# Performance work log

Measured on AMD Instinct MI355X. Metric: run time of the kernel, lower is better.

The kernel has to match this reference:

```python
import jax, jax.numpy as jnp
import numpy as np

N = 50000      # nodes
E = 800000     # edges
FEAT = 128     # input feature dim
EMB = 256      # embed_dim = heads * hid
H = 4          # attention heads
C = 64         # hid_dim per head
PED = 32       # positional encoding dim
NEG_SLOPE = 0.2


def setup_inputs() -> dict:
    key = jax.random.key(0)
    ks = jax.random.split(key, 20)
    s = lambda i, shape, sc=0.1: jax.random.normal(ks[i], shape, jnp.float32) * sc
    return {
        "x": s(0, (N, FEAT), 1.0),
        "x_masked": s(1, (N, FEAT), 1.0),
        "PE": s(2, (N, PED), 1.0),
        "PE_noise": s(3, (N, PED), 1.0),
        "edge_index": jax.random.randint(ks[4], (2, E), 0, N),
        # PEG positional encoder (linear + relu)
        "W_peg": s(5, (PED, PED)), "b_peg": jnp.zeros((PED,), jnp.float32),
        # GAT layer 0
        "W0": s(6, (FEAT, H * C)), "a_s0": s(7, (H, C)), "a_d0": s(8, (H, C)),
        "w_pe0": s(9, (H,)), "W_u0": s(10, (PED, PED)),
        # GAT layer 1
        "W1": s(11, (EMB, H * C)), "a_s1": s(12, (H, C)), "a_d1": s(13, (H, C)),
        "w_pe1": s(14, (H,)), "W_u1": s(15, (PED, PED)),
    }


def _gat(x, pe, src, dst, W, a_s, a_d, w_pe, W_u):
    # PE-aware GATConv: standard GAT attention + PE-distance bias per head.
    xp = (x @ W).reshape(-1, H, C)                       # [N,H,C]
    al_s = (xp * a_s).sum(-1)                            # [N,H]
    al_d = (xp * a_d).sum(-1)                            # [N,H]
    dist = jnp.sqrt(((pe[src] - pe[dst]) ** 2).sum(-1) + 1e-8)   # [E]
    logits = jax.nn.leaky_relu(al_s[src] + al_d[dst], NEG_SLOPE) \
             + dist[:, None] * w_pe                      # [E,H]
    # segment softmax over incoming edges of each dst node
    m = jax.ops.segment_max(logits, dst, num_segments=N)
    e = jnp.exp(logits - m[dst])
    den = jax.ops.segment_sum(e, dst, num_segments=N)
    alpha = e / (den[dst] + 1e-16)                       # [E,H]
    out = jax.ops.segment_sum(alpha[:, :, None] * xp[src], dst,
                              num_segments=N).reshape(-1, H * C)  # [N,H*C]
    pe_out = jax.nn.relu(pe @ W_u)                       # per-layer PE update
    return out, pe_out


def reference(x, x_masked, PE, PE_noise, W_peg, b_peg,
              W0, a_s0, a_d0, w_pe0, W_u0,
              W1, a_s1, a_d1, w_pe1, W_u1, edge_index):
    src, dst = edge_index[0], edge_index[1]
    # PEG encoder on both PE branches
    pe = jax.nn.relu(PE @ W_peg + b_peg)
    pe_n = jax.nn.relu(PE_noise @ W_peg + b_peg)
    # layer 0 (dual branches; eval mode -> dropout is identity)
    h, pe_n = _gat(x, pe_n, src, dst, W0, a_s0, a_d0, w_pe0, W_u0)
    hm, pe = _gat(x_masked, pe, src, dst, W0, a_s0, a_d0, w_pe0, W_u0)
    h = jax.nn.relu(h)
    hm = jax.nn.relu(hm)
    # layer 1 (last layer: no activation)
    h, pe_n = _gat(h, pe_n, src, dst, W1, a_s1, a_d1, w_pe1, W_u1)
    hm, pe = _gat(hm, pe, src, dst, W1, a_s1, a_d1, w_pe1, W_u1)
    return (hm, pe_n)
```

## Files before the change

### kernel.cpp

```cpp
#include <hip/hip_runtime.h>
#include <hip/hip_bf16.h>

#define N_NODES 50000
#define N_EDGES 800000
#define NEG_SLOPE 0.2f

typedef __hip_bfloat16 bf16;
typedef __attribute__((ext_vector_type(8))) short short8;
typedef __attribute__((ext_vector_type(4))) float f32x4;

__device__ __forceinline__ float b2f(bf16 x) { return __bfloat162float(x); }

__device__ __forceinline__ float ldsel(const void* p, size_t i, int isbf) {
  return isbf ? __bfloat162float(((const bf16*)p)[i]) : ((const float*)p)[i];
}
__device__ __forceinline__ void stsel(void* p, size_t i, int isbf, float v) {
  if (isbf) ((bf16*)p)[i] = __float2bfloat16(v);
  else ((float*)p)[i] = v;
}

__global__ void detect_kernel(const unsigned short* __restrict__ probe,
                              int* __restrict__ flag) {
  if (threadIdx.x == 0 && blockIdx.x == 0) {
    int weird = 0;
    for (int i = 0; i < 512; i += 2) {
      int ex = (probe[i] >> 7) & 0xFF;
      if (ex >= 0x85) weird++;
    }
    *flag = (weird < 8) ? 1 : 0;
  }
}

struct CvtJobs {
  const void* src[10];
  float* dst[10];
  int n[10];
};
__global__ __launch_bounds__(256) void cvt_kernel(CvtJobs jobs, const int* __restrict__ flag) {
  int isbf = *flag;
  for (int j = 0; j < 10; j++) {
    int n = jobs.n[j];
    const void* s = jobs.src[j];
    float* d = jobs.dst[j];
    for (int i = blockIdx.x * 256 + threadIdx.x; i < n; i += gridDim.x * 256)
      d[i] = ldsel(s, i, isbf);
  }
}

template <int K>
__global__ __launch_bounds__(256) void transpose_cvt_kernel(const void* __restrict__ in,
                                                            bf16* __restrict__ out,
                                                            const int* __restrict__ flag) {
  int isbf = *flag;
  int i = blockIdx.x * 256 + threadIdx.x;
  if (i >= 256 * K) return;
  int n = i / K, k = i - n * K;
  out[i] = __float2bfloat16(ldsel(in, (size_t)k * 256 + n, isbf));
}

__global__ __launch_bounds__(256) void peg_chain3(const void* __restrict__ in,
                                                  const float* __restrict__ Wpeg,
                                                  const float* __restrict__ bpeg,
                                                  const float* __restrict__ Wu0,
                                                  const float* __restrict__ Wu1,
                                                  void* out, size_t out_off,
                                                  const int* __restrict__ flag) {
  __shared__ float w1[1024], w2[1024], w3[1024];
  __shared__ float rowA[256], rowB[256];
  int isbf = *flag;
  int tid = threadIdx.x;
  int n0 = blockIdx.x * 8;
  for (int i = tid; i < 1024; i += 256) {
    w1[i] = Wpeg[i];
    w2[i] = Wu0[i];
    w3[i] = Wu1[i];
  }
  rowA[tid] = ldsel(in, (size_t)n0 * 32 + tid, isbf);
  __syncthreads();
  int col = tid & 31, ln = tid >> 5;
  float acc = bpeg[col];
#pragma unroll
  for (int j = 0; j < 32; j++) acc += rowA[ln * 32 + j] * w1[j * 32 + col];
  rowB[tid] = fmaxf(acc, 0.f);
  __syncthreads();
  acc = 0.f;
#pragma unroll
  for (int j = 0; j < 32; j++) acc += rowB[ln * 32 + j] * w2[j * 32 + col];
  rowA[tid] = fmaxf(acc, 0.f);
  __syncthreads();
  acc = 0.f;
#pragma unroll
  for (int j = 0; j < 32; j++) acc += rowA[ln * 32 + j] * w3[j * 32 + col];
  stsel(out, out_off + (size_t)n0 * 32 + tid, isbf, fmaxf(acc, 0.f));
}

__global__ __launch_bounds__(256) void peg_chain2(const void* __restrict__ in,
                                                  const float* __restrict__ Wpeg,
                                                  const float* __restrict__ bpeg,
                                                  const float* __restrict__ Wu0,
                                                  bf16* __restrict__ pe0,
                                                  bf16* __restrict__ pe1,
                                                  const int* __restrict__ flag) {
  __shared__ float w1[1024], w2[1024];
  __shared__ float rowA[256], rowB[256];
  int isbf = *flag;
  int tid = threadIdx.x;
  int n0 = blockIdx.x * 8;
  for (int i = tid; i < 1024; i += 256) {
    w1[i] = Wpeg[i];
    w2[i] = Wu0[i];
  }
  rowA[tid] = ldsel(in, (size_t)n0 * 32 + tid, isbf);
  __syncthreads();
  int col = tid & 31, ln = tid >> 5;
  float acc = bpeg[col];
#pragma unroll
  for (int j = 0; j < 32; j++) acc += rowA[ln * 32 + j] * w1[j * 32 + col];
  acc = fmaxf(acc, 0.f);
  pe0[(size_t)n0 * 32 + tid] = __float2bfloat16(acc);
  rowB[tid] = acc;
  __syncthreads();
  acc = 0.f;
#pragma unroll
  for (int j = 0; j < 32; j++) acc += rowB[ln * 32 + j] * w2[j * 32 + col];
  pe1[(size_t)n0 * 32 + tid] = __float2bfloat16(fmaxf(acc, 0.f));
}

template <int K, bool A_DUAL>
__global__ __launch_bounds__(256) void mfma_gemm(const void* __restrict__ Ap,
                                                 const bf16* __restrict__ Bt,
                                                 bf16* __restrict__ C, int M,
                                                 const float* __restrict__ a_sf,
                                                 const float* __restrict__ a_df,
                                                 float* __restrict__ al_s,
                                                 float* __restrict__ al_d,
                                                 const int* __restrict__ flag) {
  constexpr int LDK = 136;
  __shared__ short a_lds[64 * LDK];
  __shared__ short b_lds[64 * LDK];
  __shared__ float lds_al[128];
  int nrt = (M + 63) / 64;
  int bid = blockIdx.x;
  int xcd = bid & 7;
  int jj = bid >> 3;
  int col_t = jj & 3;
  int row_t = (jj >> 2) * 8 + xcd;
  if (row_t >= nrt) return;
  int isbf = A_DUAL ? *flag : 1;
  int tid = threadIdx.x;
  int row0 = row_t * 64;
  int col0 = col_t * 64;
  int lane = tid & 63;
  int wv = tid >> 6;
  int wm = (wv & 1) * 32, wn = (wv >> 1) * 32;
  int l15 = lane & 15, quad = lane >> 4;
  if (tid < 128) lds_al[tid] = 0.f;
  f32x4 acc00 = {0.f, 0.f, 0.f, 0.f}, acc01 = acc00, acc10 = acc00, acc11 = acc00;

  for (int kb = 0; kb < K; kb += 128) {
    if (kb) __syncthreads();
    for (int idx = tid; idx < 64 * 16; idx += 256) {
      int r = idx >> 4, sidx = idx & 15;
      int gr = row0 + r;
      size_t gi = (size_t)gr * K + kb + sidx * 8;
      uint4 av = make_uint4(0u, 0u, 0u, 0u);
      if (A_DUAL && !isbf) {
        if (gr < M) {
          float4 f0 = ((const float4*)Ap)[gi / 4];
          float4 f1 = ((const float4*)Ap)[gi / 4 + 1];
          union { uint4 v; bf16 h[8]; } o;
          o.h[0] = __float2bfloat16(f0.x);
          o.h[1] = __float2bfloat16(f0.y);
          o.h[2] = __float2bfloat16(f0.z);
          o.h[3] = __float2bfloat16(f0.w);
          o.h[4] = __float2bfloat16(f1.x);
          o.h[5] = __float2bfloat16(f1.y);
          o.h[6] = __float2bfloat16(f1.z);
          o.h[7] = __float2bfloat16(f1.w);
          av = o.v;
        }
      } else {
        if (gr < M) av = *(const uint4*)&((const bf16*)Ap)[gi];
      }
      *(uint4*)&a_lds[r * LDK + sidx * 8] = av;
      *(uint4*)&b_lds[r * LDK + sidx * 8] =
          *(const uint4*)&Bt[(size_t)(col0 + r) * K + kb + sidx * 8];
    }
    __syncthreads();
#pragma unroll
    for (int k0 = 0; k0 < 128; k0 += 32) {
      int ko = k0 + quad * 8;
      short8 a0 = *(const short8*)&a_lds[(wm + l15) * LDK + ko];
      short8 a1 = *(const short8*)&a_lds[(wm + 16 + l15) * LDK + ko];
      short8 b0 = *(const short8*)&b_lds[(wn + l15) * LDK + ko];
      short8 b1 = *(const short8*)&b_lds[(wn + 16 + l15) * LDK + ko];
      acc00 = __builtin_amdgcn_mfma_f32_16x16x32_bf16(a0, b0, acc00, 0, 0, 0);
      acc01 = __builtin_amdgcn_mfma_f32_16x16x32_bf16(a0, b1, acc01, 0, 0, 0);
      acc10 = __builtin_amdgcn_mfma_f32_16x16x32_bf16(a1, b0, acc10, 0, 0, 0);
      acc11 = __builtin_amdgcn_mfma_f32_16x16x32_bf16(a1, b1, acc11, 0, 0, 0);
    }
  }
  const f32x4* accs[2][2] = {{&acc00, &acc01}, {&acc10, &acc11}};
  float as0 = a_sf[col0 + wn + l15], as1 = a_sf[col0 + wn + 16 + l15];
  float ad0 = a_df[col0 + wn + l15], ad1 = a_df[col0 + wn + 16 + l15];
#pragma unroll
  for (int i = 0; i < 2; i++) {
    float sp[4], dp[4];
#pragma unroll
    for (int r = 0; r < 4; r++) {
      float v0 = (*accs[i][0])[r], v1 = (*accs[i][1])[r];
      sp[r] = v0 * as0 + v1 * as1;
      dp[r] = v0 * ad0 + v1 * ad1;
      int grow = row0 + wm + i * 16 + quad * 4 + r;
      if (grow < M) {
        C[(size_t)grow * 256 + col0 + wn + l15] = __float2bfloat16(v0);
        C[(size_t)grow * 256 + col0 + wn + 16 + l15] = __float2bfloat16(v1);
      }
    }
#pragma unroll
    for (int off = 1; off < 16; off <<= 1) {
#pragma unroll
      for (int r = 0; r < 4; r++) {
        sp[r] += __shfl_xor(sp[r], off);
        dp[r] += __shfl_xor(dp[r], off);
      }
    }
    if (l15 == 0) {
#pragma unroll
      for (int r = 0; r < 4; r++) {
        int lrow = wm + i * 16 + quad * 4 + r;
        atomicAdd(&lds_al[lrow], sp[r]);
        atomicAdd(&lds_al[64 + lrow], dp[r]);
      }
    }
  }
  __syncthreads();
  if (tid < 64 && row0 + tid < M) {
    al_s[(size_t)(row0 + tid) * 4 + col_t] = lds_al[tid];
    al_d[(size_t)(row0 + tid) * 4 + col_t] = lds_al[64 + tid];
  }
}

__global__ __launch_bounds__(256) void hist_kernel(const int* __restrict__ dst,
                                                   int* __restrict__ deg) {
  int e = blockIdx.x * 256 + threadIdx.x;
  atomicAdd(&deg[dst[e]], 1);
}

__global__ __launch_bounds__(1024) void scan1_kernel(const int* __restrict__ deg,
                                                     int* __restrict__ tmp,
                                                     int* __restrict__ bsum, int n) {
  __shared__ int wsum[16];
  int tid = threadIdx.x;
  int idx = blockIdx.x * 1024 + tid;
  int v = (idx < n) ? deg[idx] : 0;
  int incl = v;
#pragma unroll
  for (int off = 1; off < 64; off <<= 1) {
    int t = __shfl_up(incl, off);
    if ((tid & 63) >= off) incl += t;
  }
  int wid = tid >> 6;
  if ((tid & 63) == 63) wsum[wid] = incl;
  __syncthreads();
  if (tid == 0) {
    int acc = 0;
#pragma unroll
    for (int w = 0; w < 16; w++) {
      int t = wsum[w];
      wsum[w] = acc;
      acc += t;
    }
    bsum[blockIdx.x] = acc;
  }
  __syncthreads();
  if (idx < n) tmp[idx] = wsum[wid] + incl;
}

__global__ void scan2_kernel(int* __restrict__ bsum, int nb) {
  int tid = threadIdx.x;
  int v = (tid < nb) ? bsum[tid] : 0;
  int incl = v;
#pragma unroll
  for (int off = 1; off < 64; off <<= 1) {
    int t = __shfl_up(incl, off);
    if (tid >= off) incl += t;
  }
  if (tid < nb) bsum[tid] = incl - v;
}

__global__ __launch_bounds__(1024) void scan3_kernel(const int* __restrict__ tmp,
                                                     const int* __restrict__ bsum,
                                                     int* __restrict__ rowptr, int n) {
  int idx = blockIdx.x * 1024 + threadIdx.x;
  if (idx < n) rowptr[idx + 1] = tmp[idx] + bsum[blockIdx.x];
  if (idx == 0) rowptr[0] = 0;
}

__global__ __launch_bounds__(256) void fill_kernel(const int* __restrict__ src,
                                                   const int* __restrict__ dst,
                                                   const int* __restrict__ rowptr,
                                                   int* __restrict__ fill,
                                                   int* __restrict__ csr_src) {
  int e = blockIdx.x * 256 + threadIdx.x;
  int d = dst[e];
  int pos = atomicAdd(&fill[d], 1);
  csr_src[rowptr[d] + pos] = src[e];
}

template <bool RELU, bool OUT_DUAL>
__global__ __launch_bounds__(256) void agg_kernel(const bf16* __restrict__ xp,
                                                  const bf16* __restrict__ pe,
                                                  const float* __restrict__ al_s,
                                                  const float* __restrict__ al_d,
                                                  const float* __restrict__ w_pe,
                                                  const int* __restrict__ csr_src,
                                                  const int* __restrict__ rowptr,
                                                  void* out, const int* __restrict__ flag) {
  int isbf = OUT_DUAL ? *flag : 1;
  int lane = threadIdx.x & 63;
  int n = blockIdx.x * 4 + (threadIdx.x >> 6);
  int q = lane >> 4, li = lane & 15, h = li >> 2;
  unsigned int ud = *(const unsigned int*)&pe[(size_t)n * 32 + li * 2];
  float pdlo = __uint_as_float(ud << 16);
  float pdhi = __uint_as_float(ud & 0xffff0000u);
  float ald = al_d[(size_t)n * 4 + h];
  float wph = w_pe[h];
  int s1 = rowptr[n + 1];
  int s = rowptr[n] + q;
  float acc[16];
#pragma unroll
  for (int j = 0; j < 16; j++) acc[j] = 0.f;
  float asum = 0.f;

  int sn_c = -1, sn_n = -1;
  unsigned int pes_c = 0, pes_n = 0;
  float als_c = 0.f, als_n = 0.f;
  uint4 xc0 = make_uint4(0u, 0u, 0u, 0u), xc1 = xc0;
  uint4 xn0 = xc0, xn1 = xc0;
  if (s < s1) {
    sn_c = csr_src[s];
    pes_c = *(const unsigned int*)&pe[(size_t)sn_c * 32 + li * 2];
    als_c = al_s[(size_t)sn_c * 4 + h];
    const uint4* b = (const uint4*)&xp[(size_t)sn_c * 256 + li * 16];
    xc0 = b[0];
    xc1 = b[1];
    if (s + 4 < s1) sn_n = csr_src[s + 4];
  }
  int sf = s + 8;
  while (sn_c >= 0) {
    if (sn_n >= 0) {
      pes_n = *(const unsigned int*)&pe[(size_t)sn_n * 32 + li * 2];
      als_n = al_s[(size_t)sn_n * 4 + h];
      const uint4* b = (const uint4*)&xp[(size_t)sn_n * 256 + li * 16];
      xn0 = b[0];
      xn1 = b[1];
    }
    int sn_f = (sf < s1) ? csr_src[sf] : -1;
    sf += 4;
    float dx = __uint_as_float(pes_c << 16) - pdlo;
    float dy = __uint_as_float(pes_c & 0xffff0000u) - pdhi;
    float d2 = dx * dx + dy * dy;
#pragma unroll
    for (int off = 1; off < 16; off <<= 1) d2 += __shfl_xor(d2, off);
    float lg = als_c + ald;
    lg = (lg >= 0.f) ? lg : NEG_SLOPE * lg;
    lg += sqrtf(d2 + 1e-8f) * wph;
    float a = __expf(lg);
    unsigned int u[8] = {xc0.x, xc0.y, xc0.z, xc0.w, xc1.x, xc1.y, xc1.z, xc1.w};
#pragma unroll
    for (int p = 0; p < 8; p++) {
      acc[2 * p] += a * __uint_as_float(u[p] << 16);
      acc[2 * p + 1] += a * __uint_as_float(u[p] & 0xffff0000u);
    }
    asum += a;
    sn_c = sn_n;
    pes_c = pes_n;
    als_c = als_n;
    xc0 = xn0;
    xc1 = xn1;
    sn_n = sn_f;
  }
#pragma unroll
  for (int j = 0; j < 16; j++) {
    acc[j] += __shfl_xor(acc[j], 16);
    acc[j] += __shfl_xor(acc[j], 32);
  }
  asum += __shfl_xor(asum, 16);
  asum += __shfl_xor(asum, 32);
  if (q == 0) {
    float inv = 1.f / (asum + 1e-16f);
    size_t oi = (size_t)n * 256 + li * 16;
    if (OUT_DUAL && !isbf) {
      float* of = (float*)out;
#pragma unroll
      for (int p = 0; p < 4; p++) {
        float4 f;
        f.x = acc[4 * p] * inv;
        f.y = acc[4 * p + 1] * inv;
        f.z = acc[4 * p + 2] * inv;
        f.w = acc[4 * p + 3] * inv;
        if (RELU) {
          f.x = fmaxf(f.x, 0.f);
          f.y = fmaxf(f.y, 0.f);
          f.z = fmaxf(f.z, 0.f);
          f.w = fmaxf(f.w, 0.f);
        }
        *(float4*)&of[oi + 4 * p] = f;
      }
    } else {
      union { uint4 v[2]; bf16 hh[16]; } o;
#pragma unroll
      for (int j = 0; j < 16; j++) {
        float r = acc[j] * inv;
        if (RELU) r = fmaxf(r, 0.f);
        o.hh[j] = __float2bfloat16(r);
      }
      uint4* ob = (uint4*)&((bf16*)out)[oi];
      ob[0] = o.v[0];
      ob[1] = o.v[1];
    }
  }
}

extern "C" void kernel_launch(void* const* d_in, const int* in_sizes, int n_in,
                              void* d_out, int out_size, void* d_ws, size_t ws_size,
                              hipStream_t stream) {
  const void* x_masked = d_in[1];
  const void* PE = d_in[2];
  const void* PE_noise = d_in[3];
  const int* ei = (const int*)d_in[4];
  const int* src = ei;
  const int* dst = ei + N_EDGES;

  char* w = (char*)d_ws;
  auto alloc = [&](size_t bytes) -> char* {
    char* p = w;
    w += (bytes + 255) / 256 * 256;
    return p;
  };
  int* flag = (int*)alloc(4);
  float* W_peg_f = (float*)alloc(1024 * 4);
  float* b_peg_f = (float*)alloc(32 * 4);
  float* a_s0_f = (float*)alloc(256 * 4);
  float* a_d0_f = (float*)alloc(256 * 4);
  float* w_pe0_f = (float*)alloc(4 * 4);
  float* W_u0_f = (float*)alloc(1024 * 4);
  float* a_s1_f = (float*)alloc(256 * 4);
  float* a_d1_f = (float*)alloc(256 * 4);
  float* w_pe1_f = (float*)alloc(4 * 4);
  float* W_u1_f = (float*)alloc(1024 * 4);
  bf16* Wt0 = (bf16*)alloc(32768 * 2);
  bf16* Wt1 = (bf16*)alloc(65536 * 2);
  bf16* pe0_bf = (bf16*)alloc((size_t)N_NODES * 32 * 2);
  bf16* pe1_bf = (bf16*)alloc((size_t)N_NODES * 32 * 2);
  float* al_s = (float*)alloc((size_t)N_NODES * 4 * 4);
  float* al_d = (float*)alloc((size_t)N_NODES * 4 * 4);
  int* degfill = (int*)alloc((size_t)N_NODES * 2 * 4);
  int* deg = degfill;
  int* fill = degfill + N_NODES;
  int* rowptr = (int*)alloc((size_t)(N_NODES + 1) * 4);
  int* stmp = (int*)alloc((size_t)N_NODES * 4);
  int* bsum = (int*)alloc(64 * 4);
  int* csr_src = (int*)alloc((size_t)N_EDGES * 4);
  bf16* xp = (bf16*)alloc((size_t)N_NODES * 256 * 2);
  bf16* hm0 = (bf16*)alloc((size_t)N_NODES * 256 * 2);

  detect_kernel<<<1, 64, 0, stream>>>((const unsigned short*)d_in[5], flag);
  CvtJobs jobs;
  int ji = 0;
  auto addjob = [&](const void* s, float* d, int n) {
    jobs.src[ji] = s; jobs.dst[ji] = d; jobs.n[ji] = n; ji++;
  };
  addjob(d_in[5], W_peg_f, 1024);
  addjob(d_in[6], b_peg_f, 32);
  addjob(d_in[8], a_s0_f, 256);
  addjob(d_in[9], a_d0_f, 256);
  addjob(d_in[10], w_pe0_f, 4);
  addjob(d_in[11], W_u0_f, 1024);
  addjob(d_in[13], a_s1_f, 256);
  addjob(d_in[14], a_d1_f, 256);
  addjob(d_in[15], w_pe1_f, 4);
  addjob(d_in[16], W_u1_f, 1024);
  cvt_kernel<<<16, 256, 0, stream>>>(jobs, flag);
  transpose_cvt_kernel<128><<<128, 256, 0, stream>>>(d_in[7], Wt0, flag);
  transpose_cvt_kernel<256><<<256, 256, 0, stream>>>(d_in[12], Wt1, flag);

  hipMemsetAsync(degfill, 0, (size_t)N_NODES * 2 * 4, stream);

  hist_kernel<<<N_EDGES / 256, 256, 0, stream>>>(dst, deg);
  scan1_kernel<<<49, 1024, 0, stream>>>(deg, stmp, bsum, N_NODES);
  scan2_kernel<<<1, 64, 0, stream>>>(bsum, 49);
  scan3_kernel<<<49, 1024, 0, stream>>>(stmp, bsum, rowptr, N_NODES);
  fill_kernel<<<N_EDGES / 256, 256, 0, stream>>>(src, dst, rowptr, fill, csr_src);

  peg_chain3<<<N_NODES / 8, 256, 0, stream>>>(PE_noise, W_peg_f, b_peg_f, W_u0_f, W_u1_f,
                                              d_out, (size_t)N_NODES * 256, flag);
  peg_chain2<<<N_NODES / 8, 256, 0, stream>>>(PE, W_peg_f, b_peg_f, W_u0_f, pe0_bf, pe1_bf, flag);

  int nrt = (N_NODES + 63) / 64;
  int gblk = ((nrt + 7) / 8) * 8 * 4;

  mfma_gemm<128, true><<<gblk, 256, 0, stream>>>(x_masked, Wt0, xp, N_NODES,
                                                 a_s0_f, a_d0_f, al_s, al_d, flag);
  agg_kernel<true, false><<<N_NODES / 4, 256, 0, stream>>>(
      xp, pe0_bf, al_s, al_d, w_pe0_f, csr_src, rowptr, hm0, flag);

  mfma_gemm<256, false><<<gblk, 256, 0, stream>>>(hm0, Wt1, xp, N_NODES,
                                                  a_s1_f, a_d1_f, al_s, al_d, flag);
  agg_kernel<false, true><<<N_NODES / 4, 256, 0, stream>>>(
      xp, pe1_bf, al_s, al_d, w_pe1_f, csr_src, rowptr, d_out, flag);
}
```

Measured before the change: 470.3 us.

## Merge setup and PEG kernels, unroll aggregation loop two edges per step

Folds the dtype-detection, weight conversion and two transpose kernels into a single prep kernel, with each block running its own detection. The two PEG chain kernels become one launch that branches on block index. The aggregation loop now processes two edges per iteration with a double-buffered prefetch, using a -1e30 logit so out-of-range slots contribute zero weight. The goal is fewer kernel launches and more memory-level parallelism in the gather, at the cost of more registers and redundant detection work in every prep block.

```diff
diff --git a/kernel.cpp b/kernel.cpp
--- a/kernel.cpp
+++ b/kernel.cpp
@@ -19,16 +19,16 @@
   else ((float*)p)[i] = v;
 }
 
-__global__ void detect_kernel(const unsigned short* __restrict__ probe,
-                              int* __restrict__ flag) {
-  if (threadIdx.x == 0 && blockIdx.x == 0) {
-    int weird = 0;
-    for (int i = 0; i < 512; i += 2) {
-      int ex = (probe[i] >> 7) & 0xFF;
-      if (ex >= 0x85) weird++;
-    }
-    *flag = (weird < 8) ? 1 : 0;
-  }
+__device__ __forceinline__ int block_detect(const unsigned short* __restrict__ probe) {
+  __shared__ int wcount;
+  int tid = threadIdx.x;
+  if (tid == 0) wcount = 0;
+  __syncthreads();
+  int ex = (probe[2 * tid] >> 7) & 0xFF;
+  unsigned long long m = __ballot(ex >= 0x85);
+  if ((tid & 63) == 0) atomicAdd(&wcount, __popcll(m));
+  __syncthreads();
+  return wcount < 8;
 }
 
 struct CvtJobs {
@@ -36,44 +36,57 @@
   float* dst[10];
   int n[10];
 };
-__global__ __launch_bounds__(256) void cvt_kernel(CvtJobs jobs, const int* __restrict__ flag) {
-  int isbf = *flag;
-  for (int j = 0; j < 10; j++) {
-    int n = jobs.n[j];
-    const void* s = jobs.src[j];
-    float* d = jobs.dst[j];
-    for (int i = blockIdx.x * 256 + threadIdx.x; i < n; i += gridDim.x * 256)
-      d[i] = ldsel(s, i, isbf);
-  }
-}
-
-template <int K>
-__global__ __launch_bounds__(256) void transpose_cvt_kernel(const void* __restrict__ in,
-                                                            bf16* __restrict__ out,
-                                                            const int* __restrict__ flag) {
-  int isbf = *flag;
-  int i = blockIdx.x * 256 + threadIdx.x;
-  if (i >= 256 * K) return;
-  int n = i / K, k = i - n * K;
-  out[i] = __float2bfloat16(ldsel(in, (size_t)k * 256 + n, isbf));
-}
-
-__global__ __launch_bounds__(256) void peg_chain3(const void* __restrict__ in,
-                                                  const float* __restrict__ Wpeg,
-                                                  const float* __restrict__ bpeg,
-                                                  const float* __restrict__ Wu0,
-                                                  const float* __restrict__ Wu1,
-                                                  void* out, size_t out_off,
-                                                  const int* __restrict__ flag) {
+__global__ __launch_bounds__(256) void prep_kernel(CvtJobs jobs,
+                                                   const unsigned short* __restrict__ probe,
+                                                   const void* __restrict__ W0in,
+                                                   bf16* __restrict__ Wt0,
+                                                   const void* __restrict__ W1in,
+                                                   bf16* __restrict__ Wt1,
+                                                   int* __restrict__ flag) {
+  int tid = threadIdx.x;
+  int isbf = block_detect(probe);
+  int b = blockIdx.x;
+  if (b == 0 && tid == 0) *flag = isbf;
+  if (b < 16) {
+    for (int j = 0; j < 10; j++) {
+      int n = jobs.n[j];
+      const void* s = jobs.src[j];
+      float* d = jobs.dst[j];
+      for (int i = b * 256 + tid; i < n; i += 16 * 256) d[i] = ldsel(s, i, isbf);
+    }
+  } else if (b < 16 + 128) {
+    int i = (b - 16) * 256 + tid;
+    int n = i >> 7, k = i & 127;
+    Wt0[i] = __float2bfloat16(ldsel(W0in, (size_t)k * 256 + n, isbf));
+  } else {
+    int i = (b - 144) * 256 + tid;
+    int n = i >> 8, k = i & 255;
+    Wt1[i] = __float2bfloat16(ldsel(W1in, (size_t)k * 256 + n, isbf));
+  }
+}
+
+__global__ __launch_bounds__(256) void peg_all(const void* __restrict__ pen,
+                                               const void* __restrict__ pem,
+                                               const float* __restrict__ Wpeg,
+                                               const float* __restrict__ bpeg,
+                                               const float* __restrict__ Wu0,
+                                               const float* __restrict__ Wu1,
+                                               void* out, size_t out_off,
+                                               bf16* __restrict__ pe0,
+                                               bf16* __restrict__ pe1,
+                                               const int* __restrict__ flag) {
   __shared__ float w1[1024], w2[1024], w3[1024];
   __shared__ float rowA[256], rowB[256];
   int isbf = *flag;
   int tid = threadIdx.x;
-  int n0 = blockIdx.x * 8;
+  int b = blockIdx.x;
+  bool c3 = b < (N_NODES / 8);
+  int n0 = (c3 ? b : b - N_NODES / 8) * 8;
+  const void* in = c3 ? pen : pem;
   for (int i = tid; i < 1024; i += 256) {
     w1[i] = Wpeg[i];
     w2[i] = Wu0[i];
-    w3[i] = Wu1[i];
+    if (c3) w3[i] = Wu1[i];
   }
   rowA[tid] = ldsel(in, (size_t)n0 * 32 + tid, isbf);
   __syncthreads();
@@ -81,49 +94,24 @@
   float acc = bpeg[col];
 #pragma unroll
   for (int j = 0; j < 32; j++) acc += rowA[ln * 32 + j] * w1[j * 32 + col];
-  rowB[tid] = fmaxf(acc, 0.f);
+  acc = fmaxf(acc, 0.f);
+  if (!c3) pe0[(size_t)n0 * 32 + tid] = __float2bfloat16(acc);
+  rowB[tid] = acc;
   __syncthreads();
   acc = 0.f;
 #pragma unroll
   for (int j = 0; j < 32; j++) acc += rowB[ln * 32 + j] * w2[j * 32 + col];
-  rowA[tid] = fmaxf(acc, 0.f);
+  acc = fmaxf(acc, 0.f);
+  if (!c3) {
+    pe1[(size_t)n0 * 32 + tid] = __float2bfloat16(acc);
+    return;
+  }
+  rowA[tid] = acc;
   __syncthreads();
   acc = 0.f;
 #pragma unroll
   for (int j = 0; j < 32; j++) acc += rowA[ln * 32 + j] * w3[j * 32 + col];
   stsel(out, out_off + (size_t)n0 * 32 + tid, isbf, fmaxf(acc, 0.f));
-}
-
-__global__ __launch_bounds__(256) void peg_chain2(const void* __restrict__ in,
-                                                  const float* __restrict__ Wpeg,
-                                                  const float* __restrict__ bpeg,
-                                                  const float* __restrict__ Wu0,
-                                                  bf16* __restrict__ pe0,
-                                                  bf16* __restrict__ pe1,
-                                                  const int* __restrict__ flag) {
-  __shared__ float w1[1024], w2[1024];
-  __shared__ float rowA[256], rowB[256];
-  int isbf = *flag;
-  int tid = threadIdx.x;
-  int n0 = blockIdx.x * 8;
-  for (int i = tid; i < 1024; i += 256) {
-    w1[i] = Wpeg[i];
-    w2[i] = Wu0[i];
-  }
-  rowA[tid] = ldsel(in, (size_t)n0 * 32 + tid, isbf);
-  __syncthreads();
-  int col = tid & 31, ln = tid >> 5;
-  float acc = bpeg[col];
-#pragma unroll
-  for (int j = 0; j < 32; j++) acc += rowA[ln * 32 + j] * w1[j * 32 + col];
-  acc = fmaxf(acc, 0.f);
-  pe0[(size_t)n0 * 32 + tid] = __float2bfloat16(acc);
-  rowB[tid] = acc;
-  __syncthreads();
-  acc = 0.f;
-#pragma unroll
-  for (int j = 0; j < 32; j++) acc += rowB[ln * 32 + j] * w2[j * 32 + col];
-  pe1[(size_t)n0 * 32 + tid] = __float2bfloat16(fmaxf(acc, 0.f));
 }
 
 template <int K, bool A_DUAL>
@@ -326,60 +314,70 @@
   float pdhi = __uint_as_float(ud & 0xffff0000u);
   float ald = al_d[(size_t)n * 4 + h];
   float wph = w_pe[h];
-  int s1 = rowptr[n + 1];
-  int s = rowptr[n] + q;
+  int rp = rowptr[n], s1 = rowptr[n + 1];
+  int niter = (s1 - rp + 7) >> 3;
+  int s = rp + q;
   float acc[16];
 #pragma unroll
   for (int j = 0; j < 16; j++) acc[j] = 0.f;
   float asum = 0.f;
 
-  int sn_c = -1, sn_n = -1;
-  unsigned int pes_c = 0, pes_n = 0;
-  float als_c = 0.f, als_n = 0.f;
-  uint4 xc0 = make_uint4(0u, 0u, 0u, 0u), xc1 = xc0;
-  uint4 xn0 = xc0, xn1 = xc0;
-  if (s < s1) {
-    sn_c = csr_src[s];
-    pes_c = *(const unsigned int*)&pe[(size_t)sn_c * 32 + li * 2];
-    als_c = al_s[(size_t)sn_c * 4 + h];
-    const uint4* b = (const uint4*)&xp[(size_t)sn_c * 256 + li * 16];
-    xc0 = b[0];
-    xc1 = b[1];
-    if (s + 4 < s1) sn_n = csr_src[s + 4];
-  }
-  int sf = s + 8;
-  while (sn_c >= 0) {
-    if (sn_n >= 0) {
-      pes_n = *(const unsigned int*)&pe[(size_t)sn_n * 32 + li * 2];
-      als_n = al_s[(size_t)sn_n * 4 + h];
-      const uint4* b = (const uint4*)&xp[(size_t)sn_n * 256 + li * 16];
-      xn0 = b[0];
-      xn1 = b[1];
-    }
-    int sn_f = (sf < s1) ? csr_src[sf] : -1;
-    sf += 4;
-    float dx = __uint_as_float(pes_c << 16) - pdlo;
-    float dy = __uint_as_float(pes_c & 0xffff0000u) - pdhi;
+  auto LD = [&](int sn, unsigned int& pes, float& als, uint4& x0, uint4& x1) {
+    int idx = sn >= 0 ? sn : 0;
+    pes = *(const unsigned int*)&pe[(size_t)idx * 32 + li * 2];
+    float a = al_s[(size_t)idx * 4 + h];
+    als = sn >= 0 ? a : -1e30f;
+    const uint4* b = (const uint4*)&xp[(size_t)idx * 256 + li * 16];
+    x0 = b[0];
+    x1 = b[1];
+  };
+  auto COMPUTE = [&](unsigned int pes, float als, uint4 v0, uint4 v1) {
+    float dx = __uint_as_float(pes << 16) - pdlo;
+    float dy = __uint_as_float(pes & 0xffff0000u) - pdhi;
     float d2 = dx * dx + dy * dy;
 #pragma unroll
     for (int off = 1; off < 16; off <<= 1) d2 += __shfl_xor(d2, off);
-    float lg = als_c + ald;
+    float lg = als + ald;
     lg = (lg >= 0.f) ? lg : NEG_SLOPE * lg;
     lg += sqrtf(d2 + 1e-8f) * wph;
     float a = __expf(lg);
-    unsigned int u[8] = {xc0.x, xc0.y, xc0.z, xc0.w, xc1.x, xc1.y, xc1.z, xc1.w};
+    unsigned int u[8] = {v0.x, v0.y, v0.z, v0.w, v1.x, v1.y, v1.z, v1.w};
 #pragma unroll
     for (int p = 0; p < 8; p++) {
       acc[2 * p] += a * __uint_as_float(u[p] << 16);
       acc[2 * p + 1] += a * __uint_as_float(u[p] & 0xffff0000u);
     }
     asum += a;
-    sn_c = sn_n;
-    pes_c = pes_n;
-    als_c = als_n;
-    xc0 = xn0;
-    xc1 = xn1;
-    sn_n = sn_f;
+  };
+
+  int sc0 = -1, sc1 = -1, sn0 = -1, sn1 = -1;
+  unsigned int pc0 = 0, pc1 = 0, pn0 = 0, pn1 = 0;
+  float ac0 = -1e30f, ac1 = -1e30f, an0 = -1e30f, an1 = -1e30f;
+  uint4 z = make_uint4(0u, 0u, 0u, 0u);
+  uint4 xc00 = z, xc01 = z, xc10 = z, xc11 = z;
+  uint4 xn00 = z, xn01 = z, xn10 = z, xn11 = z;
+
+  if (niter > 0) {
+    sc0 = (s < s1) ? csr_src[s] : -1;
+    sc1 = (s + 4 < s1) ? csr_src[s + 4] : -1;
+    LD(sc0, pc0, ac0, xc00, xc01);
+    LD(sc1, pc1, ac1, xc10, xc11);
+    sn0 = (s + 8 < s1) ? csr_src[s + 8] : -1;
+    sn1 = (s + 12 < s1) ? csr_src[s + 12] : -1;
+  }
+  for (int t = 0; t < niter; t++) {
+    LD(sn0, pn0, an0, xn00, xn01);
+    LD(sn1, pn1, an1, xn10, xn11);
+    int sb = s + 8 * t + 16;
+    int sf0 = (sb < s1) ? csr_src[sb] : -1;
+    int sf1 = (sb + 4 < s1) ? csr_src[sb + 4] : -1;
+    COMPUTE(pc0, ac0, xc00, xc01);
+    COMPUTE(pc1, ac1, xc10, xc11);
+    sc0 = sn0; sc1 = sn1;
+    pc0 = pn0; pc1 = pn1;
+    ac0 = an0; ac1 = an1;
+    xc00 = xn00; xc01 = xn01; xc10 = xn10; xc11 = xn11;
+    sn0 = sf0; sn1 = sf1;
   }
 #pragma unroll
   for (int j = 0; j < 16; j++) {
@@ -466,7 +464,6 @@
   bf16* xp = (bf16*)alloc((size_t)N_NODES * 256 * 2);
   bf16* hm0 = (bf16*)alloc((size_t)N_NODES * 256 * 2);
 
-  detect_kernel<<<1, 64, 0, stream>>>((const unsigned short*)d_in[5], flag);
   CvtJobs jobs;
   int ji = 0;
   auto addjob = [&](const void* s, float* d, int n) {
@@ -482,9 +479,8 @@
   addjob(d_in[14], a_d1_f, 256);
   addjob(d_in[15], w_pe1_f, 4);
   addjob(d_in[16], W_u1_f, 1024);
-  cvt_kernel<<<16, 256, 0, stream>>>(jobs, flag);
-  transpose_cvt_kernel<128><<<128, 256, 0, stream>>>(d_in[7], Wt0, flag);
-  transpose_cvt_kernel<256><<<256, 256, 0, stream>>>(d_in[12], Wt1, flag);
+  prep_kernel<<<400, 256, 0, stream>>>(jobs, (const unsigned short*)d_in[5],
+                                       d_in[7], Wt0, d_in[12], Wt1, flag);
 
   hipMemsetAsync(degfill, 0, (size_t)N_NODES * 2 * 4, stream);
 
@@ -494,9 +490,10 @@
   scan3_kernel<<<49, 1024, 0, stream>>>(stmp, bsum, rowptr, N_NODES);
   fill_kernel<<<N_EDGES / 256, 256, 0, stream>>>(src, dst, rowptr, fill, csr_src);
 
-  peg_chain3<<<N_NODES / 8, 256, 0, stream>>>(PE_noise, W_peg_f, b_peg_f, W_u0_f, W_u1_f,
-                                              d_out, (size_t)N_NODES * 256, flag);
-  peg_chain2<<<N_NODES / 8, 256, 0, stream>>>(PE, W_peg_f, b_peg_f, W_u0_f, pe0_bf, pe1_bf, flag);
+  peg_all<<<2 * (N_NODES / 8), 256, 0, stream>>>(PE_noise, PE, W_peg_f, b_peg_f,
+                                                 W_u0_f, W_u1_f, d_out,
+                                                 (size_t)N_NODES * 256, pe0_bf,
+                                                 pe1_bf, flag);
 
   int nrt = (N_NODES + 63) / 64;
   int gblk = ((nrt + 7) / 8) * 8 * 4;
```

Result: faster. 458.3 us (-2.6%).
